# Kernel optimization log

Hardware: AMD Instinct MI355X
Metric: run time of the kernel (lower is better)

The kernel has to match this reference:

```python
import jax, jax.numpy as jnp
import numpy as np

N = 100000   # nodes
E = 1600000  # edges
D = 128      # input_dim
H = 128      # hidden_dim
CH = 16      # cluster_hidden_dim
P = 10       # processor_nodes


def setup_inputs() -> dict:
    key = jax.random.key(0)
    ks = jax.random.split(key, 22)
    s = 0.05
    return {
        "x": jax.random.normal(ks[0], (N, D), jnp.float32),
        "edges": jax.random.randint(ks[1], (2, E), 0, N, dtype=jnp.int32),
        "edge_attr": jax.random.uniform(ks[2], (E,), jnp.float32),
        "ready": jax.random.randint(ks[3], (N, 1), 0, 2, dtype=jnp.int32),
        "proc_emb": jax.random.normal(ks[4], (P, 3), jnp.float32),
        # GCN layers (PyG GCNConv: lin without bias, explicit bias added after aggregation)
        "gcn_w": jax.random.normal(ks[5], (2, D, H), jnp.float32) * s,
        "gcn_b": jax.random.normal(ks[6], (2, H), jnp.float32) * s,
        # listmlp: Linear(H,H) -> relu, then Linear(H,1)
        "mlp_w1": jax.random.normal(ks[7], (H, H), jnp.float32) * s,
        "mlp_b1": jax.random.normal(ks[8], (H,), jnp.float32) * s,
        "mlp_w2": jax.random.normal(ks[9], (H, 1), jnp.float32) * s,
        "mlp_b2": jax.random.normal(ks[10], (1,), jnp.float32) * s,
        # listmlp_value: Linear(H,1)
        "val_w": jax.random.normal(ks[11], (H, 1), jnp.float32) * s,
        "val_b": jax.random.normal(ks[12], (1,), jnp.float32) * s,
        # cluster_linear: Linear(3*P, CH)
        "cl_w": jax.random.normal(ks[13], (3 * P, CH), jnp.float32) * s,
        "cl_b": jax.random.normal(ks[14], (CH,), jnp.float32) * s,
        # listmlp_pass: Linear(H+CH,H) -> relu, then Linear(H,1)
        "pass_w1": jax.random.normal(ks[15], (H + CH, H), jnp.float32) * s,
        "pass_b1": jax.random.normal(ks[16], (H,), jnp.float32) * s,
        "pass_w2": jax.random.normal(ks[17], (H, 1), jnp.float32) * s,
        "pass_b2": jax.random.normal(ks[18], (1,), jnp.float32) * s,
    }


def _gcn_layer(x, row, col, w_e, W, b):
    # PyG GCNConv with flow='target_to_source': out[row] += norm_e * (x @ W)[col]
    # gcn_norm with idx=row: deg[i] = sum of edge weights with row==i (self-loops included)
    h = x @ W                                              # [N,H]
    deg = jax.ops.segment_sum(w_e, row, num_segments=N)    # [N]
    dis = jnp.where(deg > 0, jax.lax.rsqrt(deg), 0.0)      # deg^-1/2, inf -> 0
    norm = dis[row] * w_e * dis[col]                       # [E+N]
    msg = h[col] * norm[:, None]                           # [E+N,H] gather
    out = jax.ops.segment_sum(msg, row, num_segments=N)    # [N,H] scatter-add
    return out + b


def _forward(x, edges, edge_attr, ready, proc_emb, gcn_w, gcn_b,
             mlp_w1, mlp_b1, mlp_w2, mlp_b2, val_w, val_b, cl_w, cl_b,
             pass_w1, pass_b1, pass_w2, pass_b2):
    # add self-loops with weight 1 (GCNConv default add_self_loops=True)
    loop = jnp.arange(N, dtype=edges.dtype)
    row = jnp.concatenate([edges[0], loop])
    col = jnp.concatenate([edges[1], loop])
    w_e = jnp.concatenate([edge_attr, jnp.ones((N,), edge_attr.dtype)])

    h = x
    for l in range(2):
        h = jax.nn.relu(_gcn_layer(h, row, col, w_e, gcn_w[l], gcn_b[l]))

    mask = ready[:, 0] > 0                                 # [N] bool
    v = jnp.mean(h, axis=0)                                # [H]
    x_pass = jnp.max(jnp.where(mask[:, None], h, -jnp.inf), axis=0)  # masked max, [H]

    fc = proc_emb.reshape(-1) @ cl_w + cl_b                # [CH]
    x_pass = jnp.concatenate([x_pass, fc], axis=0)         # [H+CH]

    v = v @ val_w + val_b                                  # [1]

    logits = jax.nn.relu(h @ mlp_w1 + mlp_b1) @ mlp_w2 + mlp_b2        # [N,1]
    x_pass = jax.nn.relu(x_pass @ pass_w1 + pass_b1) @ pass_w2 + pass_b2  # [1]

    # torch indexes logits[ready]; here we mask non-ready entries with -inf so
    # the softmax over [N+1] matches torch's values on the ready rows.
    node_logits = jnp.where(mask, logits[:, 0], -jnp.inf)
    probs = jax.nn.softmax(jnp.concatenate([node_logits, x_pass], axis=0))  # [N+1]
    return probs, v


def reference(x, edges, edge_attr, ready, proc_emb, gcn_w, gcn_b,
              mlp_w1, mlp_b1, mlp_w2, mlp_b2, val_w, val_b, cl_w, cl_b,
              pass_w1, pass_b1, pass_w2, pass_b2):
    return _forward(x, edges, edge_attr, ready, proc_emb, gcn_w, gcn_b,
                    mlp_w1, mlp_b1, mlp_w2, mlp_b2, val_w, val_b, cl_w, cl_b,
                    pass_w1, pass_b1, pass_w2, pass_b2)
```

## Files before the change

kernel.cpp:

```cpp
#include <hip/hip_runtime.h>
#include <cstdint>

#define NN 100000
#define EE 1600000
#define HH 128
#define NREP 64
#define PSZ (NN / 8)
#define HPP (PSZ / 2)
#define SS 64
#define CAP 300000
#define NBB 500
#define BCH 3200
#define SCAN_CHUNK 512
#define NSCAN ((NN + SCAN_CHUNK - 1) / SCAN_CHUNK)

typedef unsigned long long u64;
typedef unsigned short ushort;
typedef unsigned char uchar;
typedef __attribute__((ext_vector_type(8))) short bf16x8;
typedef __attribute__((ext_vector_type(4))) float f32x4;
typedef __attribute__((ext_vector_type(2))) float f32x2;

__device__ __forceinline__ void gl2lds16(const void* g, void* l) {
#if __has_builtin(__builtin_amdgcn_global_load_lds)
    __builtin_amdgcn_global_load_lds(
        (const __attribute__((address_space(1))) unsigned int*)g,
        (__attribute__((address_space(3))) unsigned int*)l, 16, 0, 0);
#else
    *(uint4*)l = *(const uint4*)g;
#endif
}

__device__ __forceinline__ ushort f2bf(float x) {
    union { float f; unsigned u; } v; v.f = x;
    unsigned r = v.u + 0x7fffu + ((v.u >> 16) & 1u);
    return (ushort)(r >> 16);
}
__device__ __forceinline__ float bf2f(unsigned h16) {
    union { unsigned u; float f; } v; v.u = h16 << 16; return v.f;
}

__device__ __forceinline__ uchar f2fp8(float a) {
    return (uchar)(__builtin_amdgcn_cvt_pk_fp8_f32(a, a, 0, false) & 0xff);
}
__device__ __forceinline__ void unpack8_fp8(uint2 q, float* v) {
    f32x2 a = __builtin_amdgcn_cvt_pk_f32_fp8(q.x, false);
    f32x2 b = __builtin_amdgcn_cvt_pk_f32_fp8(q.x, true);
    f32x2 c = __builtin_amdgcn_cvt_pk_f32_fp8(q.y, false);
    f32x2 d = __builtin_amdgcn_cvt_pk_f32_fp8(q.y, true);
    v[0] = a[0]; v[1] = a[1]; v[2] = b[0]; v[3] = b[1];
    v[4] = c[0]; v[5] = c[1]; v[6] = d[0]; v[7] = d[1];
}

__device__ __forceinline__ unsigned encf(float f) {
    int b = __float_as_int(f);
    return (b >= 0) ? ((unsigned)b | 0x80000000u) : ~(unsigned)b;
}
__device__ __forceinline__ float decf(unsigned u) {
    return (u & 0x80000000u) ? __int_as_float((int)(u & 0x7fffffffu))
                             : __int_as_float((int)(~u));
}
#define ENC_NEG_INF 0x007FFFFFu

__global__ void k_setup(float* __restrict__ meansum, unsigned* __restrict__ maxenc,
                        unsigned* __restrict__ lmaxenc, float* __restrict__ esum,
                        int* __restrict__ gtail,
                        const float* __restrict__ w0, const float* __restrict__ w1,
                        const float* __restrict__ w2, ushort* __restrict__ wt) {
    int idx = blockIdx.x * blockDim.x + threadIdx.x;
    if (idx < NREP * HH) { meansum[idx] = 0.f; maxenc[idx] = ENC_NEG_INF; }
    if (idx < 8) gtail[idx] = 0;
    if (idx == 0) { lmaxenc[0] = ENC_NEG_INF; esum[0] = 0.f; }
    if (idx < 3 * HH * HH) {
        int mat = idx >> 14;
        int e = idx & 16383;
        int n = e >> 7, k = e & 127;
        int g = k >> 3, el = k & 7;
        const float* src = (mat == 0) ? w0 : (mat == 1) ? w1 : w2;
        int pos = (mat << 14) | (n << 7) | (((g ^ (n & 15)) << 3) | el);
        wt[pos] = f2bf(src[k * HH + n]);
    }
}

__global__ __launch_bounds__(256) void k_bucket(const int* __restrict__ rows,
                                                const int* __restrict__ cols,
                                                const float* __restrict__ ea,
                                                int* __restrict__ gtail,
                                                u64* __restrict__ ebuck) {
    __shared__ u64 buf[8][1024];
    __shared__ int cnt8[8];
    __shared__ int rsv[8];
    int t = threadIdx.x;
    if (t < 8) cnt8[t] = 0;
    __syncthreads();
    int e0 = blockIdx.x * BCH;
    int e1 = e0 + BCH;
    for (int ebase = e0; ebase < e1; ebase += 1024) {
        int e = ebase + t * 4;
        if (e < e1) {
            int4 r4 = *(const int4*)(rows + e);
            int4 c4 = *(const int4*)(cols + e);
            float4 a4 = *(const float4*)(ea + e);
            int rr[4] = {r4.x, r4.y, r4.z, r4.w};
            int cc[4] = {c4.x, c4.y, c4.z, c4.w};
            float aa[4] = {a4.x, a4.y, a4.z, a4.w};
#pragma unroll
            for (int j = 0; j < 4; ++j) {
                int p = rr[j] / PSZ;
                int rl = rr[j] - p * PSZ;
                unsigned q = (unsigned)(aa[j] * 32767.0f + 0.5f);
                u64 en = ((u64)rl << 32) | (u64)(((unsigned)cc[j] << 15) | q);
                int idx = atomicAdd(&cnt8[p], 1);
                buf[p][idx] = en;
            }
        }
        __syncthreads();
        if (t < 8) rsv[t] = atomicAdd(&gtail[t], cnt8[t]);
        __syncthreads();
#pragma unroll
        for (int p = 0; p < 8; ++p) {
            int nn = cnt8[p], oo = rsv[p];
            u64* dst = ebuck + (size_t)p * CAP + oo;
            for (int j = t; j < nn; j += 256) dst[j] = buf[p][j];
        }
        __syncthreads();
        if (t < 8) cnt8[t] = 0;
        __syncthreads();
    }
}

__global__ __launch_bounds__(256) void k_cnt2(const u64* __restrict__ ebuck,
                                              const int* __restrict__ gtail,
                                              unsigned* __restrict__ cntp) {
    __shared__ unsigned h32[HPP];
    int b = blockIdx.x;
    int s = b >> 3, p = b & 7;
    for (int j = threadIdx.x; j < HPP; j += 256) h32[j] = 0;
    __syncthreads();
    int pc = gtail[p];
    int len = (pc + SS - 1) / SS;
    int lo = s * len, hi = min(lo + len, pc);
    const u64* src = ebuck + (size_t)p * CAP;
    for (int i = lo + threadIdx.x; i < hi; i += 256) {
        int rl = (int)(src[i] >> 32);
        atomicAdd(&h32[rl >> 1], (rl & 1) ? 0x10000u : 1u);
    }
    __syncthreads();
    unsigned* dst = cntp + (size_t)(p * SS + s) * HPP;
    for (int j = threadIdx.x; j < HPP; j += 256) dst[j] = h32[j];
}

__global__ void k_cntscan(const unsigned* __restrict__ cntp, int* __restrict__ count,
                          unsigned* __restrict__ deltap, int* __restrict__ basep,
                          int* __restrict__ bsum) {
    int b = blockIdx.x, t = threadIdx.x;
    int rp = b * 256 + t;
    int c0 = 0, c1 = 0;
    if (rp < NN / 2) {
        int p = rp / HPP, j = rp - p * HPP;
        unsigned s0 = 0, s1 = 0;
#pragma unroll 8
        for (int c = 0; c < SS; ++c) {
            size_t o = (size_t)(p * SS + c) * HPP + j;
            unsigned v = cntp[o];
            deltap[o] = s0 | (s1 << 16);
            s0 += v & 0xffffu;
            s1 += v >> 16;
        }
        c0 = (int)s0; c1 = (int)s1;
        *(int2*)(count + 2 * rp) = make_int2(c0, c1);
    }
    c0 = (c0 + 7) & ~7;
    c1 = (c1 + 7) & ~7;
    int s = c0 + c1;
    int lane = t & 63, w = t >> 6;
    int v = s;
#pragma unroll
    for (int off = 1; off < 64; off <<= 1) {
        int u = __shfl_up(v, off, 64);
        if (lane >= off) v += u;
    }
    __shared__ int wsum[4];
    if (lane == 63) wsum[w] = v;
    __syncthreads();
    int wadd = 0;
    for (int j = 0; j < w; ++j) wadd += wsum[j];
    int incl = v + wadd;
    int excl = incl - s;
    int i0 = 2 * rp;
    if (i0 < NN) basep[i0] = excl;
    if (i0 + 1 < NN) basep[i0 + 1] = excl + c0;
    if (t == 255) bsum[b] = incl;
}

__global__ void k_scan2(int* __restrict__ bsum, int* __restrict__ base) {
    __shared__ int tmp[256];
    int t = threadIdx.x;
    int v = (t < NSCAN) ? bsum[t] : 0;
    tmp[t] = v;
    __syncthreads();
    for (int off = 1; off < 256; off <<= 1) {
        int u = (t >= off) ? tmp[t - off] : 0;
        __syncthreads();
        tmp[t] += u;
        __syncthreads();
    }
    if (t == NSCAN - 1) base[NN] = tmp[t];
    if (t < NSCAN) bsum[t] = tmp[t] - v;
}

__global__ __launch_bounds__(256) void k_fill2(const u64* __restrict__ ebuck,
                                               const int* __restrict__ gtail,
                                               const unsigned* __restrict__ deltap,
                                               const int* __restrict__ basep,
                                               const int* __restrict__ bsum,
                                               unsigned* __restrict__ csre) {
    __shared__ int nxt[PSZ];
    int b = blockIdx.x;
    int s = b >> 3, p = b & 7;
    const unsigned* dsrc = deltap + (size_t)(p * SS + s) * HPP;
    const int* bsrc = basep + p * PSZ;
    for (int j = threadIdx.x; j < HPP; j += 256) {
        unsigned d = dsrc[j];
        int2 bb = *(const int2*)(bsrc + 2 * j);
        int badd = bsum[(p * PSZ + 2 * j) >> 9];
        nxt[2 * j] = bb.x + badd + (int)(d & 0xffffu);
        nxt[2 * j + 1] = bb.y + badd + (int)(d >> 16);
    }
    __syncthreads();
    int pc = gtail[p];
    int len = (pc + SS - 1) / SS;
    int lo = s * len, hi = min(lo + len, pc);
    const u64* src = ebuck + (size_t)p * CAP;
    for (int i = lo + threadIdx.x; i < hi; i += 256) {
        u64 en = src[i];
        int rl = (int)(en >> 32);
        int slot = atomicAdd(&nxt[rl], 1);
        csre[slot] = (unsigned)(en & 0xffffffffu);
    }
}

__global__ void k_degsum(const int* __restrict__ count, unsigned* __restrict__ csre,
                         const int* __restrict__ basep, const int* __restrict__ bsum,
                         int* __restrict__ base, float* __restrict__ dis) {
    int r = blockIdx.x * blockDim.x + threadIdx.x;
    if (r >= NN) return;
    int lo = basep[r] + bsum[r >> 9];
    int hip = (r == NN - 1) ? base[NN] : (basep[r + 1] + bsum[(r + 1) >> 9]);
    base[r] = lo;
    int hireal = lo + count[r];
    float s = 0.f;
    for (int e = lo; e < hireal; ++e) s += (float)(csre[e] & 0x7fffu);
    unsigned selfv = (unsigned)r << 15;
    for (int e = hireal; e < hip; ++e) csre[e] = selfv;
    dis[r] = rsqrtf(1.0f + s * (1.0f / 32767.0f));
}

__global__ __launch_bounds__(256) void k_gather(const uchar* __restrict__ hW,
                                                const unsigned* __restrict__ csre,
                                                const int* __restrict__ base,
                                                const float* __restrict__ dis,
                                                const float* __restrict__ bias,
                                                ushort* __restrict__ agg) {
    int node = blockIdx.x * 16 + (threadIdx.x >> 4);
    if (node >= NN) return;
    int l = threadIdx.x & 15;
    int f = l * 8;
    int lo = base[node], hi = base[node + 1];
    float disn = dis[node];
    float wk = disn * (1.0f / 32767.0f);
    float acc[8];
    {
        uint2 q = *(const uint2*)(hW + (size_t)node * HH + f);
        float v[8]; unpack8_fp8(q, v);
#pragma unroll
        for (int j = 0; j < 8; ++j) acc[j] = disn * v[j];
    }
    for (int eb = lo; eb < hi; eb += 8) {
        uint4 pa = *(const uint4*)(csre + eb);
        uint4 pb = *(const uint4*)(csre + eb + 4);
        unsigned pp[8] = {pa.x, pa.y, pa.z, pa.w, pb.x, pb.y, pb.z, pb.w};
        uint2 qq[8];
#pragma unroll
        for (int j = 0; j < 8; ++j)
            qq[j] = *(const uint2*)(hW + (size_t)(pp[j] >> 15) * HH + f);
#pragma unroll
        for (int j = 0; j < 8; ++j) {
            float w = (float)(pp[j] & 0x7fffu) * wk;
            float v[8]; unpack8_fp8(qq[j], v);
#pragma unroll
            for (int k = 0; k < 8; ++k) acc[k] += w * v[k];
        }
    }
    float4 b0 = *(const float4*)(bias + f);
    float4 b1 = *(const float4*)(bias + f + 4);
    ushort o[8];
    o[0] = f2bf(fmaxf(acc[0] + b0.x, 0.f)); o[1] = f2bf(fmaxf(acc[1] + b0.y, 0.f));
    o[2] = f2bf(fmaxf(acc[2] + b0.z, 0.f)); o[3] = f2bf(fmaxf(acc[3] + b0.w, 0.f));
    o[4] = f2bf(fmaxf(acc[4] + b1.x, 0.f)); o[5] = f2bf(fmaxf(acc[5] + b1.y, 0.f));
    o[6] = f2bf(fmaxf(acc[6] + b1.z, 0.f)); o[7] = f2bf(fmaxf(acc[7] + b1.w, 0.f));
    int gsw = (l ^ (node & 15)) * 8;
    *(uint4*)(agg + (size_t)node * HH + gsw) = *(uint4*)o;
}

template <int MODE>
__global__ __launch_bounds__(256) void k_mfma(const void* __restrict__ Ain,
                                              const ushort* __restrict__ Wt,
                                              uchar* __restrict__ C,
                                              const float* __restrict__ dis,
                                              const float* __restrict__ b1,
                                              const float* __restrict__ w2v,
                                              const float* __restrict__ b2,
                                              const int* __restrict__ ready,
                                              float* __restrict__ logits,
                                              float* __restrict__ meansum,
                                              unsigned* __restrict__ maxenc,
                                              unsigned* __restrict__ lmaxenc, int n) {
    __shared__ __align__(16) ushort As[64 * HH];
    __shared__ ushort Ws[128 * HH];
    __shared__ int rdy[64];
    __shared__ float xs[128];
    __shared__ float xmf[128];
    __shared__ unsigned slmax;
    const int t = threadIdx.x;
    const int rb = blockIdx.x * 64;
    const int wv = t >> 6, ln = t & 63;

    {
        const char* wsb = (const char*)Wt;
        char* wdb = (char*)Ws;
#pragma unroll
        for (int i = 0; i < 8; ++i) {
            int blk = wv * 8 + i;
            gl2lds16(wsb + blk * 1024 + ln * 16, wdb + blk * 1024);
        }
    }
    if (MODE != 0) {
        const char* asb = (const char*)Ain + (size_t)rb * HH * 2;
        char* adb = (char*)As;
#pragma unroll
        for (int i = 0; i < 4; ++i) {
            int blk = wv * 4 + i;
            gl2lds16(asb + blk * 1024 + ln * 16, adb + blk * 1024);
        }
    } else {
#pragma unroll
        for (int i = 0; i < 4; ++i) {
            int m = i * 16 + (t >> 4);
            int k = (t & 15) * 8;
            ushort pk[8];
            const float* Af = (const float*)Ain;
            float4 v0 = make_float4(0.f, 0.f, 0.f, 0.f), v1 = v0;
            if (rb + m < n) {
                const float* src = Af + (size_t)(rb + m) * HH + k;
                v0 = *(const float4*)src;
                v1 = *(const float4*)(src + 4);
            }
            pk[0] = f2bf(v0.x); pk[1] = f2bf(v0.y); pk[2] = f2bf(v0.z); pk[3] = f2bf(v0.w);
            pk[4] = f2bf(v1.x); pk[5] = f2bf(v1.y); pk[6] = f2bf(v1.z); pk[7] = f2bf(v1.w);
            int gsw = (t & 15) ^ (m & 15);
            *(uint4*)(As + m * HH + gsw * 8) = *(uint4*)pk;
        }
    }
    if (MODE == 2) {
        if (t < 64) rdy[t] = (rb + t < n) ? ready[rb + t] : 0;
        if (t == 0) slmax = ENC_NEG_INF;
    }
    __syncthreads();

    const int cl = ln & 15;
    const int kq = ln >> 4;
    const int m0 = wv * 16;

    f32x4 acc[8];
#pragma unroll
    for (int c = 0; c < 8; ++c) acc[c] = (f32x4){0.f, 0.f, 0.f, 0.f};

#pragma unroll
    for (int kk = 0; kk < 4; ++kk) {
        int g = kk * 4 + kq;
        bf16x8 bfr = *(const bf16x8*)(As + (m0 + cl) * HH + ((g ^ cl) * 8));
#pragma unroll
        for (int c = 0; c < 8; ++c) {
            bf16x8 afr = *(const bf16x8*)(Ws + (c * 16 + cl) * HH + ((g ^ cl) * 8));
            acc[c] = __builtin_amdgcn_mfma_f32_16x16x32_bf16(afr, bfr, acc[c], 0, 0, 0);
        }
    }

    const int node = rb + m0 + cl;
    if (MODE < 2) {
        float d = (node < n) ? dis[node] : 0.f;
        uchar* Cs = (uchar*)As;
        __syncthreads();
#pragma unroll
        for (int c = 0; c < 8; ++c) {
            unsigned u = __builtin_amdgcn_cvt_pk_fp8_f32(acc[c][0] * d, acc[c][1] * d, 0u, false);
            u = __builtin_amdgcn_cvt_pk_fp8_f32(acc[c][2] * d, acc[c][3] * d, u, true);
            *(unsigned*)(Cs + (m0 + cl) * 144 + c * 16 + kq * 4) = u;
        }
        __syncthreads();
        int row = t >> 2, off = (t & 3) * 32;
        if (rb + row < n) {
            uint4 q0 = *(const uint4*)(Cs + row * 144 + off);
            uint4 q1 = *(const uint4*)(Cs + row * 144 + off + 16);
            uchar* dst = C + (size_t)(rb + row) * HH + off;
            *(uint4*)dst = q0;
            *(uint4*)(dst + 16) = q1;
        }
    } else {
        float s = 0.f;
#pragma unroll
        for (int c = 0; c < 8; ++c) {
            float4 bb = *(const float4*)(b1 + c * 16 + kq * 4);
            float4 ww = *(const float4*)(w2v + c * 16 + kq * 4);
            s += fmaxf(acc[c][0] + bb.x, 0.f) * ww.x;
            s += fmaxf(acc[c][1] + bb.y, 0.f) * ww.y;
            s += fmaxf(acc[c][2] + bb.z, 0.f) * ww.z;
            s += fmaxf(acc[c][3] + bb.w, 0.f) * ww.w;
        }
        s += __shfl_xor(s, 16, 64);
        s += __shfl_xor(s, 32, 64);
        unsigned mylmax = ENC_NEG_INF;
        if (kq == 0 && node < n) {
            float lg = s + b2[0];
            logits[node] = lg;
            if (rdy[m0 + cl] > 0) mylmax = encf(lg);
        }
        if (mylmax != ENC_NEG_INF) atomicMax(&slmax, mylmax);

        int lim = min(64, n - rb);
        {
            int f = t & 127, h = t >> 7;
            int gf = f >> 3, fo = f & 7;
            float sum = 0.f, mx = -3.4e38f;
            int mlo = h * 32, mhi = min(lim, mlo + 32);
            for (int m = mlo; m < mhi; ++m) {
                float v = bf2f(As[m * HH + ((gf ^ (m & 15)) * 8) + fo]);
                sum += v;
                if (rdy[m] > 0) mx = fmaxf(mx, v);
            }
            if (h == 0) { xs[f] = sum; xmf[f] = mx; }
            __syncthreads();
            if (h == 1) {
                sum += xs[f];
                mx = fmaxf(mx, xmf[f]);
                int rep = blockIdx.x & (NREP - 1);
                atomicAdd(&meansum[rep * HH + f], sum);
                if (mx > -3.0e38f) atomicMax(&maxenc[rep * HH + f], encf(mx));
            }
        }
        __syncthreads();
        if (t == 0 && slmax != ENC_NEG_INF) atomicMax(lmaxenc, slmax);
    }
}

__global__ void k_fin1(const float* __restrict__ meansum, const unsigned* __restrict__ maxenc,
                       const unsigned* __restrict__ lmaxenc,
                       const float* __restrict__ val_w, const float* __restrict__ val_b,
                       const float* __restrict__ pe, const float* __restrict__ cl_w,
                       const float* __restrict__ cl_b, const float* __restrict__ pw1,
                       const float* __restrict__ pb1, const float* __restrict__ pw2,
                       const float* __restrict__ pb2, float* __restrict__ scal,
                       float* __restrict__ d_out) {
    __shared__ float xp[144];
    __shared__ float msum[HH];
    __shared__ float zp[HH];
    int t = threadIdx.x;
    if (t < HH) {
        float s = 0.f;
        unsigned mx = ENC_NEG_INF;
        for (int r = 0; r < NREP; ++r) {
            s += meansum[r * HH + t];
            unsigned e = maxenc[r * HH + t];
            if (e > mx) mx = e;
        }
        msum[t] = s;
        xp[t] = decf(mx);
    } else if (t < 144) {
        int c = t - HH;
        float s = cl_b[c];
        for (int k = 0; k < 30; ++k) s += pe[k] * cl_w[k * 16 + c];
        xp[t] = s;
    }
    __syncthreads();
    if (t < HH) {
        float s = pb1[t];
        for (int k = 0; k < 144; ++k) s += xp[k] * pw1[k * HH + t];
        zp[t] = fmaxf(s, 0.f);
    }
    __syncthreads();
    if (t < 64) {
        float s1 = zp[t] * pw2[t] + zp[t + 64] * pw2[t + 64];
        float s2 = msum[t] * val_w[t] + msum[t + 64] * val_w[t + 64];
#pragma unroll
        for (int off = 32; off > 0; off >>= 1) {
            s1 += __shfl_xor(s1, off, 64);
            s2 += __shfl_xor(s2, off, 64);
        }
        if (t == 0) {
            float xpass = s1 + pb2[0];
            float v = s2 * (1.0f / NN) + val_b[0];
            float M = fmaxf(decf(lmaxenc[0]), xpass);
            scal[0] = M;
            scal[1] = expf(xpass - M);
            d_out[NN + 1] = v;
        }
    }
}

__global__ __launch_bounds__(256) void k_exp(const float* __restrict__ logits,
                                             const int* __restrict__ ready,
                                             const float* __restrict__ scal,
                                             float* __restrict__ d_out,
                                             float* __restrict__ esum) {
    __shared__ float warr[4];
    int t = threadIdx.x;
    int i = blockIdx.x * 256 + t;
    float M = scal[0];
    float p = 0.f;
    if (i < NN) {
        if (ready[i] > 0) p = expf(logits[i] - M);
        d_out[i] = p;
    }
    float s = p;
#pragma unroll
    for (int off = 32; off > 0; off >>= 1) s += __shfl_xor(s, off, 64);
    if ((t & 63) == 0) warr[t >> 6] = s;
    __syncthreads();
    if (t == 0) atomicAdd(esum, warr[0] + warr[1] + warr[2] + warr[3]);
}

__global__ void k_scale(const float* __restrict__ esum, const float* __restrict__ scal,
                        float* __restrict__ d_out) {
    int i = blockIdx.x * blockDim.x + threadIdx.x;
    float inv = 1.0f / (esum[0] + scal[1]);
    if (i < NN) d_out[i] *= inv;
    else if (i == NN) d_out[NN] = scal[1] * inv;
}

extern "C" void kernel_launch(void* const* d_in, const int* in_sizes, int n_in,
                              void* d_out, int out_size, void* d_ws, size_t ws_size,
                              hipStream_t stream) {
    const float* x      = (const float*)d_in[0];
    const int*   edges  = (const int*)d_in[1];
    const float* eattr  = (const float*)d_in[2];
    const int*   ready  = (const int*)d_in[3];
    const float* pe     = (const float*)d_in[4];
    const float* gcn_w  = (const float*)d_in[5];
    const float* gcn_b  = (const float*)d_in[6];
    const float* mlp_w1 = (const float*)d_in[7];
    const float* mlp_b1 = (const float*)d_in[8];
    const float* mlp_w2 = (const float*)d_in[9];
    const float* mlp_b2 = (const float*)d_in[10];
    const float* val_w  = (const float*)d_in[11];
    const float* val_b  = (const float*)d_in[12];
    const float* cl_w   = (const float*)d_in[13];
    const float* cl_b   = (const float*)d_in[14];
    const float* pw1    = (const float*)d_in[15];
    const float* pb1    = (const float*)d_in[16];
    const float* pw2    = (const float*)d_in[17];
    const float* pb2    = (const float*)d_in[18];

    const int* rows = edges;
    const int* cols = edges + EE;

    char* P = (char*)d_ws;
    size_t off = 0;
    auto carve = [&](size_t bytes) {
        off = (off + 255) & ~(size_t)255;
        void* p = P + off;
        off += bytes;
        return p;
    };
    float* dis     = (float*)carve(NN * 4);
    float* logits  = (float*)carve(NN * 4);
    int*   count   = (int*)carve(NN * 4);
    int*   basep   = (int*)carve(NN * 4);
    int*   base    = (int*)carve((NN + 1) * 4);
    int*   bsum    = (int*)carve(256 * 4);
    ushort* bufB   = (ushort*)carve((size_t)NN * HH * 2);
    uchar* bufH    = (uchar*)carve((size_t)NN * HH);
    unsigned* csre = (unsigned*)carve((size_t)(EE + 8 * NN) * 4);
    u64*   ebuck   = (u64*)carve((size_t)8 * CAP * 8);
    float* meansum = (float*)carve(NREP * HH * 4);
    unsigned* maxenc = (unsigned*)carve(NREP * HH * 4);
    unsigned* lmaxenc = (unsigned*)carve(4);
    float* esum    = (float*)carve(4);
    float* scal    = (float*)carve(8);
    int*   gtail   = (int*)carve(8 * 4);
    ushort* wt     = (ushort*)carve(3 * HH * HH * 2);

    unsigned* cntp   = (unsigned*)bufB;
    unsigned* deltap = (unsigned*)bufB + (size_t)8 * SS * HPP;

    float* out = (float*)d_out;

    const int nb = (NN + 255) / 256;
    const int gb = (NN + 63) / 64;
    const int ab = (NN + 15) / 16;
    const int pb = 8 * SS;

    k_setup<<<(3 * HH * HH + 255) / 256, 256, 0, stream>>>(meansum, maxenc, lmaxenc, esum,
                                                           gtail, gcn_w, gcn_w + HH * HH,
                                                           mlp_w1, wt);

    k_bucket<<<NBB, 256, 0, stream>>>(rows, cols, eattr, gtail, ebuck);
    k_cnt2<<<pb, 256, 0, stream>>>(ebuck, gtail, cntp);
    k_cntscan<<<NSCAN, 256, 0, stream>>>(cntp, count, deltap, basep, bsum);
    k_scan2<<<1, 256, 0, stream>>>(bsum, base);
    k_fill2<<<pb, 256, 0, stream>>>(ebuck, gtail, deltap, basep, bsum, csre);
    k_degsum<<<nb, 256, 0, stream>>>(count, csre, basep, bsum, base, dis);

    k_mfma<0><<<gb, 256, 0, stream>>>(x, wt, bufH, dis, nullptr, nullptr, nullptr, nullptr,
                                      nullptr, nullptr, nullptr, nullptr, NN);
    k_gather<<<ab, 256, 0, stream>>>(bufH, csre, base, dis, gcn_b, bufB);

    k_mfma<1><<<gb, 256, 0, stream>>>(bufB, wt + HH * HH, bufH, dis, nullptr, nullptr, nullptr,
                                      nullptr, nullptr, nullptr, nullptr, nullptr, NN);
    k_gather<<<ab, 256, 0, stream>>>(bufH, csre, base, dis, gcn_b + HH, bufB);

    k_mfma<2><<<gb, 256, 0, stream>>>(bufB, wt + 2 * HH * HH, nullptr, nullptr, mlp_b1, mlp_w2,
                                      mlp_b2, ready, logits, meansum, maxenc, lmaxenc, NN);
    k_fin1<<<1, 256, 0, stream>>>(meansum, maxenc, lmaxenc, val_w, val_b, pe, cl_w, cl_b,
                                  pw1, pb1, pw2, pb2, scal, out);
    k_exp<<<nb, 256, 0, stream>>>(logits, ready, scal, out, esum);
    k_scale<<<(NN + 1 + 255) / 256, 256, 0, stream>>>(esum, scal, out);
}
```

Before: 330.6 us.

## Process four row tiles per MFMA block with double-buffered async A loads

Each k_mfma block now loops over four 64-row tiles, loading the 128x128 weight tile into LDS once per block instead of once per tile. In modes 1 and 2 the next A tile is prefetched into a second LDS buffer while the current one is computed. bufB gains padding so the prefetch past the last row stays in bounds. The cost is fewer blocks (less parallelism across CUs), more LDS per block (lower occupancy), and extra barriers per iteration.

```diff
diff --git a/kernel.cpp b/kernel.cpp
--- a/kernel.cpp
+++ b/kernel.cpp
@@ -13,6 +13,7 @@
 #define BCH 3200
 #define SCAN_CHUNK 512
 #define NSCAN ((NN + SCAN_CHUNK - 1) / SCAN_CHUNK)
+#define TPB 4
 
 typedef unsigned long long u64;
 typedef unsigned short ushort;
@@ -316,14 +317,14 @@
                                               float* __restrict__ meansum,
                                               unsigned* __restrict__ maxenc,
                                               unsigned* __restrict__ lmaxenc, int n) {
-    __shared__ __align__(16) ushort As[64 * HH];
     __shared__ ushort Ws[128 * HH];
+    __shared__ __align__(16) ushort As[2][64 * HH];
+    __shared__ __align__(16) uchar Cs[64 * 144];
     __shared__ int rdy[64];
     __shared__ float xs[128];
     __shared__ float xmf[128];
     __shared__ unsigned slmax;
     const int t = threadIdx.x;
-    const int rb = blockIdx.x * 64;
     const int wv = t >> 6, ln = t & 63;
 
     {
@@ -336,122 +337,136 @@
         }
     }
     if (MODE != 0) {
-        const char* asb = (const char*)Ain + (size_t)rb * HH * 2;
-        char* adb = (char*)As;
+        const char* asb = (const char*)Ain + (size_t)(blockIdx.x * TPB) * 64 * HH * 2;
+        char* adb = (char*)As[0];
 #pragma unroll
         for (int i = 0; i < 4; ++i) {
             int blk = wv * 4 + i;
             gl2lds16(asb + blk * 1024 + ln * 16, adb + blk * 1024);
         }
-    } else {
-#pragma unroll
-        for (int i = 0; i < 4; ++i) {
-            int m = i * 16 + (t >> 4);
-            int k = (t & 15) * 8;
-            ushort pk[8];
-            const float* Af = (const float*)Ain;
-            float4 v0 = make_float4(0.f, 0.f, 0.f, 0.f), v1 = v0;
-            if (rb + m < n) {
-                const float* src = Af + (size_t)(rb + m) * HH + k;
-                v0 = *(const float4*)src;
-                v1 = *(const float4*)(src + 4);
-            }
-            pk[0] = f2bf(v0.x); pk[1] = f2bf(v0.y); pk[2] = f2bf(v0.z); pk[3] = f2bf(v0.w);
-            pk[4] = f2bf(v1.x); pk[5] = f2bf(v1.y); pk[6] = f2bf(v1.z); pk[7] = f2bf(v1.w);
-            int gsw = (t & 15) ^ (m & 15);
-            *(uint4*)(As + m * HH + gsw * 8) = *(uint4*)pk;
-        }
-    }
-    if (MODE == 2) {
-        if (t < 64) rdy[t] = (rb + t < n) ? ready[rb + t] : 0;
-        if (t == 0) slmax = ENC_NEG_INF;
-    }
+    }
+    if (MODE == 2 && t == 0) slmax = ENC_NEG_INF;
     __syncthreads();
 
     const int cl = ln & 15;
     const int kq = ln >> 4;
     const int m0 = wv * 16;
 
-    f32x4 acc[8];
-#pragma unroll
-    for (int c = 0; c < 8; ++c) acc[c] = (f32x4){0.f, 0.f, 0.f, 0.f};
-
-#pragma unroll
-    for (int kk = 0; kk < 4; ++kk) {
-        int g = kk * 4 + kq;
-        bf16x8 bfr = *(const bf16x8*)(As + (m0 + cl) * HH + ((g ^ cl) * 8));
-#pragma unroll
-        for (int c = 0; c < 8; ++c) {
-            bf16x8 afr = *(const bf16x8*)(Ws + (c * 16 + cl) * HH + ((g ^ cl) * 8));
-            acc[c] = __builtin_amdgcn_mfma_f32_16x16x32_bf16(afr, bfr, acc[c], 0, 0, 0);
-        }
-    }
-
-    const int node = rb + m0 + cl;
-    if (MODE < 2) {
-        float d = (node < n) ? dis[node] : 0.f;
-        uchar* Cs = (uchar*)As;
-        __syncthreads();
-#pragma unroll
-        for (int c = 0; c < 8; ++c) {
-            unsigned u = __builtin_amdgcn_cvt_pk_fp8_f32(acc[c][0] * d, acc[c][1] * d, 0u, false);
-            u = __builtin_amdgcn_cvt_pk_fp8_f32(acc[c][2] * d, acc[c][3] * d, u, true);
-            *(unsigned*)(Cs + (m0 + cl) * 144 + c * 16 + kq * 4) = u;
-        }
-        __syncthreads();
-        int row = t >> 2, off = (t & 3) * 32;
-        if (rb + row < n) {
-            uint4 q0 = *(const uint4*)(Cs + row * 144 + off);
-            uint4 q1 = *(const uint4*)(Cs + row * 144 + off + 16);
-            uchar* dst = C + (size_t)(rb + row) * HH + off;
-            *(uint4*)dst = q0;
-            *(uint4*)(dst + 16) = q1;
-        }
-    } else {
-        float s = 0.f;
-#pragma unroll
-        for (int c = 0; c < 8; ++c) {
-            float4 bb = *(const float4*)(b1 + c * 16 + kq * 4);
-            float4 ww = *(const float4*)(w2v + c * 16 + kq * 4);
-            s += fmaxf(acc[c][0] + bb.x, 0.f) * ww.x;
-            s += fmaxf(acc[c][1] + bb.y, 0.f) * ww.y;
-            s += fmaxf(acc[c][2] + bb.z, 0.f) * ww.z;
-            s += fmaxf(acc[c][3] + bb.w, 0.f) * ww.w;
-        }
-        s += __shfl_xor(s, 16, 64);
-        s += __shfl_xor(s, 32, 64);
-        unsigned mylmax = ENC_NEG_INF;
-        if (kq == 0 && node < n) {
-            float lg = s + b2[0];
-            logits[node] = lg;
-            if (rdy[m0 + cl] > 0) mylmax = encf(lg);
-        }
-        if (mylmax != ENC_NEG_INF) atomicMax(&slmax, mylmax);
-
-        int lim = min(64, n - rb);
-        {
-            int f = t & 127, h = t >> 7;
-            int gf = f >> 3, fo = f & 7;
-            float sum = 0.f, mx = -3.4e38f;
-            int mlo = h * 32, mhi = min(lim, mlo + 32);
-            for (int m = mlo; m < mhi; ++m) {
-                float v = bf2f(As[m * HH + ((gf ^ (m & 15)) * 8) + fo]);
-                sum += v;
-                if (rdy[m] > 0) mx = fmaxf(mx, v);
-            }
-            if (h == 0) { xs[f] = sum; xmf[f] = mx; }
+    for (int tt = 0; tt < TPB; ++tt) {
+        const int rb = (blockIdx.x * TPB + tt) * 64;
+        const ushort* Asc = As[MODE == 0 ? 0 : (tt & 1)];
+
+        if (MODE == 0) {
+#pragma unroll
+            for (int i = 0; i < 4; ++i) {
+                int m = i * 16 + (t >> 4);
+                int k = (t & 15) * 8;
+                ushort pk[8];
+                const float* Af = (const float*)Ain;
+                float4 v0 = make_float4(0.f, 0.f, 0.f, 0.f), v1 = v0;
+                if (rb + m < n) {
+                    const float* src = Af + (size_t)(rb + m) * HH + k;
+                    v0 = *(const float4*)src;
+                    v1 = *(const float4*)(src + 4);
+                }
+                pk[0] = f2bf(v0.x); pk[1] = f2bf(v0.y); pk[2] = f2bf(v0.z); pk[3] = f2bf(v0.w);
+                pk[4] = f2bf(v1.x); pk[5] = f2bf(v1.y); pk[6] = f2bf(v1.z); pk[7] = f2bf(v1.w);
+                int gsw = (t & 15) ^ (m & 15);
+                *(uint4*)(As[0] + m * HH + gsw * 8) = *(uint4*)pk;
+            }
+        } else if (tt + 1 < TPB) {
+            const char* asb = (const char*)Ain + (size_t)(rb + 64) * HH * 2;
+            char* adb = (char*)As[(tt + 1) & 1];
+#pragma unroll
+            for (int i = 0; i < 4; ++i) {
+                int blk = wv * 4 + i;
+                gl2lds16(asb + blk * 1024 + ln * 16, adb + blk * 1024);
+            }
+        }
+        if (MODE == 2) {
+            if (t < 64) rdy[t] = (rb + t < n) ? ready[rb + t] : 0;
+        }
+        __syncthreads();
+
+        f32x4 acc[8];
+#pragma unroll
+        for (int c = 0; c < 8; ++c) acc[c] = (f32x4){0.f, 0.f, 0.f, 0.f};
+
+#pragma unroll
+        for (int kk = 0; kk < 4; ++kk) {
+            int g = kk * 4 + kq;
+            bf16x8 bfr = *(const bf16x8*)(Asc + (m0 + cl) * HH + ((g ^ cl) * 8));
+#pragma unroll
+            for (int c = 0; c < 8; ++c) {
+                bf16x8 afr = *(const bf16x8*)(Ws + (c * 16 + cl) * HH + ((g ^ cl) * 8));
+                acc[c] = __builtin_amdgcn_mfma_f32_16x16x32_bf16(afr, bfr, acc[c], 0, 0, 0);
+            }
+        }
+
+        const int node = rb + m0 + cl;
+        if (MODE < 2) {
+            float d = (node < n) ? dis[node] : 0.f;
+#pragma unroll
+            for (int c = 0; c < 8; ++c) {
+                unsigned u = __builtin_amdgcn_cvt_pk_fp8_f32(acc[c][0] * d, acc[c][1] * d, 0u, false);
+                u = __builtin_amdgcn_cvt_pk_fp8_f32(acc[c][2] * d, acc[c][3] * d, u, true);
+                *(unsigned*)(Cs + (m0 + cl) * 144 + c * 16 + kq * 4) = u;
+            }
             __syncthreads();
-            if (h == 1) {
-                sum += xs[f];
-                mx = fmaxf(mx, xmf[f]);
-                int rep = blockIdx.x & (NREP - 1);
-                atomicAdd(&meansum[rep * HH + f], sum);
-                if (mx > -3.0e38f) atomicMax(&maxenc[rep * HH + f], encf(mx));
-            }
-        }
-        __syncthreads();
-        if (t == 0 && slmax != ENC_NEG_INF) atomicMax(lmaxenc, slmax);
-    }
+            int row = t >> 2, off = (t & 3) * 32;
+            if (rb + row < n) {
+                uint4 q0 = *(const uint4*)(Cs + row * 144 + off);
+                uint4 q1 = *(const uint4*)(Cs + row * 144 + off + 16);
+                uchar* dst = C + (size_t)(rb + row) * HH + off;
+                *(uint4*)dst = q0;
+                *(uint4*)(dst + 16) = q1;
+            }
+        } else {
+            float s = 0.f;
+#pragma unroll
+            for (int c = 0; c < 8; ++c) {
+                float4 bb = *(const float4*)(b1 + c * 16 + kq * 4);
+                float4 ww = *(const float4*)(w2v + c * 16 + kq * 4);
+                s += fmaxf(acc[c][0] + bb.x, 0.f) * ww.x;
+                s += fmaxf(acc[c][1] + bb.y, 0.f) * ww.y;
+                s += fmaxf(acc[c][2] + bb.z, 0.f) * ww.z;
+                s += fmaxf(acc[c][3] + bb.w, 0.f) * ww.w;
+            }
+            s += __shfl_xor(s, 16, 64);
+            s += __shfl_xor(s, 32, 64);
+            unsigned mylmax = ENC_NEG_INF;
+            if (kq == 0 && node < n) {
+                float lg = s + b2[0];
+                logits[node] = lg;
+                if (rdy[m0 + cl] > 0) mylmax = encf(lg);
+            }
+            if (mylmax != ENC_NEG_INF) atomicMax(&slmax, mylmax);
+
+            int lim = min(64, n - rb);
+            {
+                int f = t & 127, h = t >> 7;
+                int gf = f >> 3, fo = f & 7;
+                float sum = 0.f, mx = -3.4e38f;
+                int mlo = h * 32, mhi = min(lim, mlo + 32);
+                for (int m = mlo; m < mhi; ++m) {
+                    float v = bf2f(Asc[m * HH + ((gf ^ (m & 15)) * 8) + fo]);
+                    sum += v;
+                    if (rdy[m] > 0) mx = fmaxf(mx, v);
+                }
+                if (h == 0) { xs[f] = sum; xmf[f] = mx; }
+                __syncthreads();
+                if (h == 1 && lim > 0) {
+                    sum += xs[f];
+                    mx = fmaxf(mx, xmf[f]);
+                    int rep = blockIdx.x & (NREP - 1);
+                    atomicAdd(&meansum[rep * HH + f], sum);
+                    if (mx > -3.0e38f) atomicMax(&maxenc[rep * HH + f], encf(mx));
+                }
+            }
+        }
+        __syncthreads();
+    }
+    if (MODE == 2 && t == 0 && slmax != ENC_NEG_INF) atomicMax(lmaxenc, slmax);
 }
 
 __global__ void k_fin1(const float* __restrict__ meansum, const unsigned* __restrict__ maxenc,
@@ -578,7 +593,7 @@
     int*   basep   = (int*)carve(NN * 4);
     int*   base    = (int*)carve((NN + 1) * 4);
     int*   bsum    = (int*)carve(256 * 4);
-    ushort* bufB   = (ushort*)carve((size_t)NN * HH * 2);
+    ushort* bufB   = (ushort*)carve((size_t)(NN + 256) * HH * 2);
     uchar* bufH    = (uchar*)carve((size_t)NN * HH);
     unsigned* csre = (unsigned*)carve((size_t)(EE + 8 * NN) * 4);
     u64*   ebuck   = (u64*)carve((size_t)8 * CAP * 8);
@@ -596,7 +611,7 @@
     float* out = (float*)d_out;
 
     const int nb = (NN + 255) / 256;
-    const int gb = (NN + 63) / 64;
+    const int gb4 = (NN + TPB * 64 - 1) / (TPB * 64);
     const int ab = (NN + 15) / 16;
     const int pb = 8 * SS;
 
@@ -611,16 +626,16 @@
     k_fill2<<<pb, 256, 0, stream>>>(ebuck, gtail, deltap, basep, bsum, csre);
     k_degsum<<<nb, 256, 0, stream>>>(count, csre, basep, bsum, base, dis);
 
-    k_mfma<0><<<gb, 256, 0, stream>>>(x, wt, bufH, dis, nullptr, nullptr, nullptr, nullptr,
-                                      nullptr, nullptr, nullptr, nullptr, NN);
+    k_mfma<0><<<gb4, 256, 0, stream>>>(x, wt, bufH, dis, nullptr, nullptr, nullptr, nullptr,
+                                       nullptr, nullptr, nullptr, nullptr, NN);
     k_gather<<<ab, 256, 0, stream>>>(bufH, csre, base, dis, gcn_b, bufB);
 
-    k_mfma<1><<<gb, 256, 0, stream>>>(bufB, wt + HH * HH, bufH, dis, nullptr, nullptr, nullptr,
-                                      nullptr, nullptr, nullptr, nullptr, nullptr, NN);
+    k_mfma<1><<<gb4, 256, 0, stream>>>(bufB, wt + HH * HH, bufH, dis, nullptr, nullptr, nullptr,
+                                       nullptr, nullptr, nullptr, nullptr, nullptr, NN);
     k_gather<<<ab, 256, 0, stream>>>(bufH, csre, base, dis, gcn_b + HH, bufB);
 
-    k_mfma<2><<<gb, 256, 0, stream>>>(bufB, wt + 2 * HH * HH, nullptr, nullptr, mlp_b1, mlp_w2,
-                                      mlp_b2, ready, logits, meansum, maxenc, lmaxenc, NN);
+    k_mfma<2><<<gb4, 256, 0, stream>>>(bufB, wt + 2 * HH * HH, nullptr, nullptr, mlp_b1, mlp_w2,
+                                       mlp_b2, ready, logits, meansum, maxenc, lmaxenc, NN);
     k_fin1<<<1, 256, 0, stream>>>(meansum, maxenc, lmaxenc, val_w, val_b, pe, cl_w, cl_b,
                                   pw1, pb1, pw2, pb2, scal, out);
     k_exp<<<nb, 256, 0, stream>>>(logits, ready, scal, out, esum);
```

Result: no change. 333.3 us (+0.8%).
